# Kernel tuning notes

Measured on AMD Instinct MI355X. Metric: run time of the kernel, lower is better.

Reference implementation:

```python
import jax, jax.numpy as jnp
import numpy as np

EPS = 1e-12  # F.normalize default eps


def _l2norm(x):
    n = jnp.linalg.norm(x, axis=-1, keepdims=True)
    return x / jnp.maximum(n, EPS)


def _group_pool(x):
    # x: (b, 4, C) row-normalized features; per-group attention pooling.
    # s_i = sum_j x_i . x_j ; weights = softmax_i(s) ; pooled = sum_i w_i x_i
    s = jnp.einsum('bic,bjc->bi', x, x)          # (b, 4)
    w = jax.nn.softmax(s, axis=1)                 # (b, 4)
    return jnp.einsum('bi,bic->bc', w, x)         # (b, C)


def setup_inputs() -> dict:
    key = jax.random.key(0)
    k1, k2 = jax.random.split(key)
    N, C = 16384, 1024
    x1 = jax.random.normal(k1, (N, C), dtype=jnp.float32)
    x2 = jax.random.normal(k2, (N, C), dtype=jnp.float32)
    return {"x1": x1, "x2": x2}


def reference(x1, x2):
    b = x2.shape[0] // 4
    C = x1.shape[1]
    x1n = _l2norm(x1).reshape(b, 4, C)
    x2n = _l2norm(x2).reshape(b, 4, C)
    p1 = _l2norm(_group_pool(x1n))                # (b, C)
    p2 = _l2norm(_group_pool(x2n))                # (b, C)
    center_loss = jnp.mean(jnp.linalg.norm(p1 - p2, axis=1))
    sim = p1 @ p2.T                               # (b, b)
    diag = jnp.arange(b)
    # cross_entropy(sim, arange) and cross_entropy(sim.T, arange)
    loss_t = -jnp.mean(jax.nn.log_softmax(sim, axis=1)[diag, diag])
    loss_i = -jnp.mean(jax.nn.log_softmax(sim, axis=0)[diag, diag])
    return (loss_t + loss_i + center_loss, p1, p2)
```

## Files before the change

kernel.cpp:

```cpp
#include <hip/hip_runtime.h>
#include <hip/hip_bf16.h>

#define BGRP 4096
#define CDIM 1024

typedef __attribute__((ext_vector_type(8))) short bf16x8;
typedef __attribute__((ext_vector_type(4))) float f32x4;
typedef __attribute__((ext_vector_type(4))) unsigned short u16x4;

__device__ __forceinline__ unsigned short f2bf(float x) {
    __hip_bfloat16 h = __float2bfloat16(x);
    unsigned short u;
    __builtin_memcpy(&u, &h, 2);
    return u;
}

__device__ __forceinline__ void gload16(const void* g, void* l) {
    __builtin_amdgcn_global_load_lds(
        (const __attribute__((address_space(1))) unsigned int*)g,
        (__attribute__((address_space(3))) unsigned int*)l, 16, 0, 0);
}

__device__ __forceinline__ void group_coefs(const float* d, float* coef) {
    float D[4][4];
    int c = 0;
    #pragma unroll
    for (int i = 0; i < 4; ++i)
        #pragma unroll
        for (int j = i; j < 4; ++j) { D[i][j] = d[c]; D[j][i] = d[c]; ++c; }
    float inv[4];
    #pragma unroll
    for (int i = 0; i < 4; ++i) inv[i] = 1.0f / fmaxf(sqrtf(D[i][i]), 1e-12f);
    float s[4];
    #pragma unroll
    for (int i = 0; i < 4; ++i) {
        float si = 0.f;
        #pragma unroll
        for (int j = 0; j < 4; ++j) si += D[i][j] * inv[i] * inv[j];
        s[i] = si;
    }
    float m = fmaxf(fmaxf(s[0], s[1]), fmaxf(s[2], s[3]));
    float e[4], se = 0.f;
    #pragma unroll
    for (int i = 0; i < 4; ++i) { e[i] = expf(s[i] - m); se += e[i]; }
    float rse = 1.0f / se;
    #pragma unroll
    for (int i = 0; i < 4; ++i) coef[i] = e[i] * rse * inv[i];
}

__device__ __forceinline__ float wave_allsum(float t) {
    t += __shfl_xor(t, 1, 64);
    t += __shfl_xor(t, 2, 64);
    t += __shfl_xor(t, 4, 64);
    t += __shfl_xor(t, 8, 64);
    t += __shfl_xor(t, 16, 64);
    t += __shfl_xor(t, 32, 64);
    return t;
}

__global__ __launch_bounds__(256, 4) void pool_kernel(
    const float* __restrict__ x1, const float* __restrict__ x2,
    float* __restrict__ out,
    unsigned short* __restrict__ p1b, unsigned short* __restrict__ p2b,
    float* __restrict__ diag, float* __restrict__ centerArr)
{
    __shared__ float plds[2][CDIM];
    const int l    = threadIdx.x & 63;
    const int wv   = threadIdx.x >> 6;
    const int gi   = wv >> 1;
    const int isx2 = wv & 1;
    const int g    = blockIdx.x * 2 + gi;

    const float* __restrict__ x = isx2 ? x2 : x1;

    float4 a[4][4];
    #pragma unroll
    for (int i = 0; i < 4; ++i)
        #pragma unroll
        for (int w = 0; w < 4; ++w)
            a[i][w] = reinterpret_cast<const float4*>(x)[(size_t)(4 * g + i) * 256 + w * 64 + l];

    float dd[10];
    {
        int c = 0;
        #pragma unroll
        for (int i = 0; i < 4; ++i)
            #pragma unroll
            for (int j = i; j < 4; ++j) {
                float s0 = 0.f;
                #pragma unroll
                for (int w = 0; w < 4; ++w)
                    s0 += a[i][w].x * a[j][w].x + a[i][w].y * a[j][w].y
                        + a[i][w].z * a[j][w].z + a[i][w].w * a[j][w].w;
                dd[c++] = s0;
            }
    }
    #pragma unroll
    for (int v = 0; v < 10; ++v) dd[v] = wave_allsum(dd[v]);

    float coef[4];
    group_coefs(dd, coef);

    float D[4][4];
    {
        int c = 0;
        #pragma unroll
        for (int i = 0; i < 4; ++i)
            #pragma unroll
            for (int j = i; j < 4; ++j) { D[i][j] = dd[c]; D[j][i] = dd[c]; ++c; }
    }
    float n = 0.f;
    #pragma unroll
    for (int i = 0; i < 4; ++i) {
        float ti = 0.f;
        #pragma unroll
        for (int j = 0; j < 4; ++j) ti += D[i][j] * coef[j];
        n += coef[i] * ti;
    }
    const float inv = 1.0f / fmaxf(sqrtf(n), 1e-12f);

    float* pout = out + 1 + (size_t)(g + (isx2 ? BGRP : 0)) * CDIM;
    unsigned short* pb = isx2 ? (p2b ? p2b + (size_t)g * CDIM : nullptr)
                              : (p1b ? p1b + (size_t)g * CDIM : nullptr);

    float4 q[4];
    #pragma unroll
    for (int w = 0; w < 4; ++w) {
        float4 qq;
        qq.x = coef[0]*a[0][w].x + coef[1]*a[1][w].x + coef[2]*a[2][w].x + coef[3]*a[3][w].x;
        qq.y = coef[0]*a[0][w].y + coef[1]*a[1][w].y + coef[2]*a[2][w].y + coef[3]*a[3][w].y;
        qq.z = coef[0]*a[0][w].z + coef[1]*a[1][w].z + coef[2]*a[2][w].z + coef[3]*a[3][w].z;
        qq.w = coef[0]*a[0][w].w + coef[1]*a[1][w].w + coef[2]*a[2][w].w + coef[3]*a[3][w].w;
        qq.x *= inv; qq.y *= inv; qq.z *= inv; qq.w *= inv;
        q[w] = qq;
    }

    if (!isx2) {
        #pragma unroll
        for (int w = 0; w < 4; ++w)
            *reinterpret_cast<float4*>(&plds[gi][w * 256 + l * 4]) = q[w];
    }

    #pragma unroll
    for (int w = 0; w < 4; ++w) {
        const int e = w * 256 + l * 4;
        pout[e + 0] = q[w].x; pout[e + 1] = q[w].y;
        pout[e + 2] = q[w].z; pout[e + 3] = q[w].w;
        if (pb != nullptr) {
            u16x4 wb;
            wb[0] = f2bf(q[w].x); wb[1] = f2bf(q[w].y);
            wb[2] = f2bf(q[w].z); wb[3] = f2bf(q[w].w);
            *reinterpret_cast<u16x4*>(pb + e) = wb;
        }
    }

    __syncthreads();

    if (isx2) {
        float dp = 0.f;
        #pragma unroll
        for (int w = 0; w < 4; ++w) {
            float4 p1v = *reinterpret_cast<const float4*>(&plds[gi][w * 256 + l * 4]);
            dp += p1v.x * q[w].x + p1v.y * q[w].y + p1v.z * q[w].z + p1v.w * q[w].w;
        }
        dp = wave_allsum(dp);
        if (l == 0) {
            diag[g] = dp;
            centerArr[g] = sqrtf(fmaxf(2.0f - 2.0f * dp, 0.0f));
        }
    }
}

__global__ __launch_bounds__(256, 4) void sim_lds_kernel(
    const unsigned short* __restrict__ p1b, const unsigned short* __restrict__ p2b,
    float* __restrict__ rowsum, float* __restrict__ colsum)
{
    __shared__ __align__(16) unsigned char lds[32768];
    const int tid  = threadIdx.x;
    const int lane = tid & 63;
    const int wid  = tid >> 6;
    const int wm = wid >> 1, wn = wid & 1;
    const int row0 = blockIdx.y * 128;
    const int col0 = blockIdx.x * 128;
    const int lr  = lane & 15;
    const int lkb = lane >> 4;

    const int srow = lane >> 3;
    const int scol = ((lane & 7) ^ srow) << 4;
    const int ch0  = wid * 4;

    f32x4 acc[4][4];
    #pragma unroll
    for (int mi = 0; mi < 4; ++mi)
        #pragma unroll
        for (int ni = 0; ni < 4; ++ni) {
            acc[mi][ni][0] = 0.f; acc[mi][ni][1] = 0.f;
            acc[mi][ni][2] = 0.f; acc[mi][ni][3] = 0.f;
        }

    const char* A = (const char*)p1b;
    const char* B = (const char*)p2b;

    for (int kt = 0; kt < 16; ++kt) {
        const size_t kbyte = (size_t)kt * 128;
        #pragma unroll
        for (int c = 0; c < 4; ++c) {
            const int chunk = ch0 + c;
            const int r = chunk * 8 + srow;
            gload16(A + (size_t)(row0 + r) * 2048 + kbyte + scol, lds + chunk * 1024);
            gload16(B + (size_t)(col0 + r) * 2048 + kbyte + scol, lds + 16384 + chunk * 1024);
        }
        __syncthreads();

        #pragma unroll
        for (int ks = 0; ks < 2; ++ks) {
            bf16x8 af[4], bg[4];
            const int cbase = (ks * 64 + lkb * 16) ^ ((lr & 7) << 4);
            #pragma unroll
            for (int i = 0; i < 4; ++i) {
                const int ra = wm * 64 + i * 16 + lr;
                const int rb = wn * 64 + i * 16 + lr;
                af[i] = *reinterpret_cast<const bf16x8*>(lds + ra * 128 + cbase);
                bg[i] = *reinterpret_cast<const bf16x8*>(lds + 16384 + rb * 128 + cbase);
            }
            #pragma unroll
            for (int mi = 0; mi < 4; ++mi)
                #pragma unroll
                for (int ni = 0; ni < 4; ++ni)
                    acc[mi][ni] = __builtin_amdgcn_mfma_f32_16x16x32_bf16(
                        af[mi], bg[ni], acc[mi][ni], 0, 0, 0);
        }
        __syncthreads();
    }

    float rs[4][4];
    float cs[4] = {0.f, 0.f, 0.f, 0.f};
    #pragma unroll
    for (int mi = 0; mi < 4; ++mi)
        #pragma unroll
        for (int r = 0; r < 4; ++r) rs[mi][r] = 0.f;

    #pragma unroll
    for (int mi = 0; mi < 4; ++mi)
        #pragma unroll
        for (int ni = 0; ni < 4; ++ni)
            #pragma unroll
            for (int r = 0; r < 4; ++r) {
                float e = __expf(acc[mi][ni][r]);
                rs[mi][r] += e;
                cs[ni] += e;
            }

    const int wrow0 = row0 + wm * 64;
    const int wcol0 = col0 + wn * 64;
    #pragma unroll
    for (int mi = 0; mi < 4; ++mi)
        #pragma unroll
        for (int r = 0; r < 4; ++r) {
            float v = rs[mi][r];
            v += __shfl_xor(v, 1, 64);
            v += __shfl_xor(v, 2, 64);
            v += __shfl_xor(v, 4, 64);
            v += __shfl_xor(v, 8, 64);
            if (lr == 0) atomicAdd(&rowsum[wrow0 + mi * 16 + lkb * 4 + r], v);
        }
    #pragma unroll
    for (int ni = 0; ni < 4; ++ni) {
        float v = cs[ni];
        v += __shfl_xor(v, 16, 64);
        v += __shfl_xor(v, 32, 64);
        if (lkb == 0) atomicAdd(&colsum[wcol0 + ni * 16 + lr], v);
    }
}

__device__ __forceinline__ bf16x8 frag_from_f32(const float* p) {
    bf16x8 r;
    #pragma unroll
    for (int i = 0; i < 8; ++i) {
        unsigned int b = __float_as_uint(p[i]);
        b += 0x7fffu + ((b >> 16) & 1u);
        r[i] = (short)(b >> 16);
    }
    return r;
}

__global__ __launch_bounds__(256) void sim_fallback_kernel(
    const float* __restrict__ p1f, const float* __restrict__ p2f,
    float* __restrict__ rowsum, float* __restrict__ colsum)
{
    const int lane = threadIdx.x & 63;
    const int wid  = threadIdx.x >> 6;
    const int wm = wid >> 1, wn = wid & 1;
    const int row0 = blockIdx.y * 128 + wm * 64;
    const int col0 = blockIdx.x * 128 + wn * 64;
    const int lr  = lane & 15;
    const int lkb = lane >> 4;
    const int lk  = lkb * 8;

    f32x4 acc[4][4];
    #pragma unroll
    for (int mi = 0; mi < 4; ++mi)
        #pragma unroll
        for (int ni = 0; ni < 4; ++ni) {
            acc[mi][ni][0] = 0.f; acc[mi][ni][1] = 0.f;
            acc[mi][ni][2] = 0.f; acc[mi][ni][3] = 0.f;
        }

    const size_t abase = (size_t)(row0 + lr) * CDIM + lk;
    const size_t bbase = (size_t)(col0 + lr) * CDIM + lk;

    for (int k = 0; k < CDIM; k += 32) {
        bf16x8 af[4], bfr[4];
        #pragma unroll
        for (int i = 0; i < 4; ++i) {
            af[i]  = frag_from_f32(p1f + abase + (size_t)i * 16 * CDIM + k);
            bfr[i] = frag_from_f32(p2f + bbase + (size_t)i * 16 * CDIM + k);
        }
        #pragma unroll
        for (int mi = 0; mi < 4; ++mi)
            #pragma unroll
            for (int ni = 0; ni < 4; ++ni)
                acc[mi][ni] = __builtin_amdgcn_mfma_f32_16x16x32_bf16(
                    af[mi], bfr[ni], acc[mi][ni], 0, 0, 0);
    }

    float rs[4][4];
    float cs[4] = {0.f, 0.f, 0.f, 0.f};
    #pragma unroll
    for (int mi = 0; mi < 4; ++mi)
        #pragma unroll
        for (int r = 0; r < 4; ++r) rs[mi][r] = 0.f;

    #pragma unroll
    for (int mi = 0; mi < 4; ++mi)
        #pragma unroll
        for (int ni = 0; ni < 4; ++ni)
            #pragma unroll
            for (int r = 0; r < 4; ++r) {
                float e = __expf(acc[mi][ni][r]);
                rs[mi][r] += e;
                cs[ni] += e;
            }

    #pragma unroll
    for (int mi = 0; mi < 4; ++mi)
        #pragma unroll
        for (int r = 0; r < 4; ++r) {
            float v = rs[mi][r];
            v += __shfl_xor(v, 1, 64);
            v += __shfl_xor(v, 2, 64);
            v += __shfl_xor(v, 4, 64);
            v += __shfl_xor(v, 8, 64);
            if (lr == 0) atomicAdd(&rowsum[row0 + mi * 16 + lkb * 4 + r], v);
        }
    #pragma unroll
    for (int ni = 0; ni < 4; ++ni) {
        float v = cs[ni];
        v += __shfl_xor(v, 16, 64);
        v += __shfl_xor(v, 32, 64);
        if (lkb == 0) atomicAdd(&colsum[col0 + ni * 16 + lr], v);
    }
}

__global__ __launch_bounds__(256) void loss_kernel(
    const float* __restrict__ rowsum, const float* __restrict__ colsum,
    const float* __restrict__ diag, const float* __restrict__ centerArr,
    float* __restrict__ out)
{
    float part = 0.f;
    for (int i = threadIdx.x; i < BGRP; i += 256)
        part += logf(rowsum[i]) + logf(colsum[i]) - 2.0f * diag[i] + centerArr[i];
    #pragma unroll
    for (int off = 32; off > 0; off >>= 1) part += __shfl_down(part, off, 64);
    __shared__ float l4[4];
    if ((threadIdx.x & 63) == 0) l4[threadIdx.x >> 6] = part;
    __syncthreads();
    if (threadIdx.x == 0)
        out[0] = (l4[0] + l4[1] + l4[2] + l4[3]) * (1.0f / (float)BGRP);
}

extern "C" void kernel_launch(void* const* d_in, const int* in_sizes, int n_in,
                              void* d_out, int out_size, void* d_ws, size_t ws_size,
                              hipStream_t stream)
{
    const float* x1 = (const float*)d_in[0];
    const float* x2 = (const float*)d_in[1];
    float* out = (float*)d_out;

    float* rowsum    = (float*)d_ws;
    float* colsum    = rowsum + BGRP;
    float* diag      = colsum + BGRP;
    float* centerArr = diag + BGRP;
    const size_t head_floats = 4 * (size_t)BGRP;
    unsigned short* p1b = (unsigned short*)((char*)d_ws + head_floats * sizeof(float));
    unsigned short* p2b = p1b + (size_t)BGRP * CDIM;
    const size_t need = head_floats * sizeof(float) + (size_t)2 * BGRP * CDIM * sizeof(unsigned short);
    const bool use_ws = (ws_size >= need);

    hipMemsetAsync(d_ws, 0, 2 * (size_t)BGRP * sizeof(float), stream);

    pool_kernel<<<BGRP / 2, 256, 0, stream>>>(x1, x2, out,
                                              use_ws ? p1b : nullptr,
                                              use_ws ? p2b : nullptr,
                                              diag, centerArr);

    dim3 gridB(BGRP / 128, BGRP / 128);
    if (use_ws) {
        sim_lds_kernel<<<gridB, 256, 0, stream>>>(p1b, p2b, rowsum, colsum);
    } else {
        sim_fallback_kernel<<<gridB, 256, 0, stream>>>(out + 1, out + 1 + (size_t)BGRP * CDIM,
                                                       rowsum, colsum);
    }

    loss_kernel<<<1, 256, 0, stream>>>(rowsum, colsum, diag, centerArr, out);
}
```

Baseline: 86.23 us.

## Replace sim GEMM with 256x256 tile, 4-deep LDS ring pipelined kernel

Swaps the 128x128 single-buffered similarity GEMM for a 512-thread, 256x256-tile kernel that keeps a 4-slot LDS ring with two stages of global loads in flight, raising MFMA priority during compute. It also folds the rowsum/colsum memset into the pool kernel, makes the fp32 pooled-output stores nontemporal, and switches logf to __logf. The larger tiles reduce global reloads, and the prefetching hides load latency. The cost is much higher LDS use (128KB per block) and fewer blocks (256) for the device. The unswizzled 64-byte LDS rows may also cause bank conflicts.

```diff
diff --git a/kernel.cpp b/kernel.cpp
--- a/kernel.cpp
+++ b/kernel.cpp
@@ -62,8 +62,12 @@
     const float* __restrict__ x1, const float* __restrict__ x2,
     float* __restrict__ out,
     unsigned short* __restrict__ p1b, unsigned short* __restrict__ p2b,
-    float* __restrict__ diag, float* __restrict__ centerArr)
+    float* __restrict__ diag, float* __restrict__ centerArr,
+    float* __restrict__ zero8k)
 {
+    if (threadIdx.x < 4)
+        zero8k[blockIdx.x * 4 + threadIdx.x] = 0.f;
+
     __shared__ float plds[2][CDIM];
     const int l    = threadIdx.x & 63;
     const int wv   = threadIdx.x >> 6;
@@ -144,8 +148,10 @@
     #pragma unroll
     for (int w = 0; w < 4; ++w) {
         const int e = w * 256 + l * 4;
-        pout[e + 0] = q[w].x; pout[e + 1] = q[w].y;
-        pout[e + 2] = q[w].z; pout[e + 3] = q[w].w;
+        __builtin_nontemporal_store(q[w].x, pout + e + 0);
+        __builtin_nontemporal_store(q[w].y, pout + e + 1);
+        __builtin_nontemporal_store(q[w].z, pout + e + 2);
+        __builtin_nontemporal_store(q[w].w, pout + e + 3);
         if (pb != nullptr) {
             u16x4 wb;
             wb[0] = f2bf(q[w].x); wb[1] = f2bf(q[w].y);
@@ -171,105 +177,120 @@
     }
 }
 
-__global__ __launch_bounds__(256, 4) void sim_lds_kernel(
+__global__ __launch_bounds__(512, 2) void sim_ring_kernel(
     const unsigned short* __restrict__ p1b, const unsigned short* __restrict__ p2b,
     float* __restrict__ rowsum, float* __restrict__ colsum)
 {
-    __shared__ __align__(16) unsigned char lds[32768];
+    __shared__ __align__(16) unsigned char lds[131072];
     const int tid  = threadIdx.x;
     const int lane = tid & 63;
     const int wid  = tid >> 6;
-    const int wm = wid >> 1, wn = wid & 1;
-    const int row0 = blockIdx.y * 128;
-    const int col0 = blockIdx.x * 128;
-    const int lr  = lane & 15;
-    const int lkb = lane >> 4;
-
-    const int srow = lane >> 3;
-    const int scol = ((lane & 7) ^ srow) << 4;
-    const int ch0  = wid * 4;
-
-    f32x4 acc[4][4];
-    #pragma unroll
-    for (int mi = 0; mi < 4; ++mi)
-        #pragma unroll
-        for (int ni = 0; ni < 4; ++ni) {
-            acc[mi][ni][0] = 0.f; acc[mi][ni][1] = 0.f;
-            acc[mi][ni][2] = 0.f; acc[mi][ni][3] = 0.f;
-        }
+    const int wm   = wid >> 2;
+    const int wn   = wid & 3;
+    const int lr   = lane & 15;
+    const int lkb  = lane >> 4;
+    const int row0 = blockIdx.y * 256;
+    const int col0 = blockIdx.x * 256;
+
+    const int srow  = wid * 16 + (lane >> 2);
+    const int scolb = (lane & 3) * 16;
 
     const char* A = (const char*)p1b;
     const char* B = (const char*)p2b;
 
-    for (int kt = 0; kt < 16; ++kt) {
-        const size_t kbyte = (size_t)kt * 128;
-        #pragma unroll
-        for (int c = 0; c < 4; ++c) {
-            const int chunk = ch0 + c;
-            const int r = chunk * 8 + srow;
-            gload16(A + (size_t)(row0 + r) * 2048 + kbyte + scol, lds + chunk * 1024);
-            gload16(B + (size_t)(col0 + r) * 2048 + kbyte + scol, lds + 16384 + chunk * 1024);
-        }
-        __syncthreads();
-
-        #pragma unroll
-        for (int ks = 0; ks < 2; ++ks) {
-            bf16x8 af[4], bg[4];
-            const int cbase = (ks * 64 + lkb * 16) ^ ((lr & 7) << 4);
-            #pragma unroll
-            for (int i = 0; i < 4; ++i) {
-                const int ra = wm * 64 + i * 16 + lr;
-                const int rb = wn * 64 + i * 16 + lr;
-                af[i] = *reinterpret_cast<const bf16x8*>(lds + ra * 128 + cbase);
-                bg[i] = *reinterpret_cast<const bf16x8*>(lds + 16384 + rb * 128 + cbase);
+    f32x4 acc[8][4];
+    #pragma unroll
+    for (int m = 0; m < 8; ++m)
+        #pragma unroll
+        for (int n = 0; n < 4; ++n) {
+            acc[m][n][0] = 0.f; acc[m][n][1] = 0.f;
+            acc[m][n][2] = 0.f; acc[m][n][3] = 0.f;
+        }
+
+    #define STAGE(T, BUF) do {                                                  \
+        const size_t kb_ = (size_t)(T) * 64;                                    \
+        char* bb_ = (char*)lds + (BUF) * 32768;                                 \
+        _Pragma("unroll")                                                       \
+        for (int r_ = 0; r_ < 2; ++r_)                                          \
+            gload16(A + (size_t)(row0 + r_ * 128 + srow) * 2048 + kb_ + scolb,  \
+                    bb_ + r_ * 8192 + wid * 1024 + lane * 16);                  \
+        _Pragma("unroll")                                                       \
+        for (int r_ = 0; r_ < 2; ++r_)                                          \
+            gload16(B + (size_t)(col0 + r_ * 128 + srow) * 2048 + kb_ + scolb,  \
+                    bb_ + 16384 + r_ * 8192 + wid * 1024 + lane * 16);          \
+    } while (0)
+
+    STAGE(0, 0);
+    STAGE(1, 1);
+
+    for (int t = 0; t < 32; ++t) {
+        if (t < 31) { asm volatile("s_waitcnt vmcnt(4)" ::: "memory"); }
+        else        { asm volatile("s_waitcnt vmcnt(0)" ::: "memory"); }
+        __builtin_amdgcn_sched_barrier(0);
+        __builtin_amdgcn_s_barrier();
+
+        if (t + 2 < 32) STAGE(t + 2, (t + 2) & 3);
+
+        const char* bb = (const char*)lds + (t & 3) * 32768;
+        bf16x8 af[8], bg[4];
+        #pragma unroll
+        for (int m = 0; m < 8; ++m)
+            af[m] = *reinterpret_cast<const bf16x8*>(
+                bb + (wm * 128 + m * 16 + lr) * 64 + lkb * 16);
+        #pragma unroll
+        for (int n = 0; n < 4; ++n)
+            bg[n] = *reinterpret_cast<const bf16x8*>(
+                bb + 16384 + (wn * 64 + n * 16 + lr) * 64 + lkb * 16);
+
+        __builtin_amdgcn_s_barrier();
+        __builtin_amdgcn_s_setprio(1);
+        #pragma unroll
+        for (int m = 0; m < 8; ++m)
+            #pragma unroll
+            for (int n = 0; n < 4; ++n)
+                acc[m][n] = __builtin_amdgcn_mfma_f32_16x16x32_bf16(
+                    af[m], bg[n], acc[m][n], 0, 0, 0);
+        __builtin_amdgcn_s_setprio(0);
+    }
+    #undef STAGE
+
+    float rs[8][4];
+    float cs[4] = {0.f, 0.f, 0.f, 0.f};
+    #pragma unroll
+    for (int m = 0; m < 8; ++m)
+        #pragma unroll
+        for (int rr = 0; rr < 4; ++rr) rs[m][rr] = 0.f;
+
+    #pragma unroll
+    for (int m = 0; m < 8; ++m)
+        #pragma unroll
+        for (int n = 0; n < 4; ++n)
+            #pragma unroll
+            for (int rr = 0; rr < 4; ++rr) {
+                float e = __expf(acc[m][n][rr]);
+                rs[m][rr] += e;
+                cs[n] += e;
             }
-            #pragma unroll
-            for (int mi = 0; mi < 4; ++mi)
-                #pragma unroll
-                for (int ni = 0; ni < 4; ++ni)
-                    acc[mi][ni] = __builtin_amdgcn_mfma_f32_16x16x32_bf16(
-                        af[mi], bg[ni], acc[mi][ni], 0, 0, 0);
-        }
-        __syncthreads();
-    }
-
-    float rs[4][4];
-    float cs[4] = {0.f, 0.f, 0.f, 0.f};
-    #pragma unroll
-    for (int mi = 0; mi < 4; ++mi)
-        #pragma unroll
-        for (int r = 0; r < 4; ++r) rs[mi][r] = 0.f;
-
-    #pragma unroll
-    for (int mi = 0; mi < 4; ++mi)
-        #pragma unroll
-        for (int ni = 0; ni < 4; ++ni)
-            #pragma unroll
-            for (int r = 0; r < 4; ++r) {
-                float e = __expf(acc[mi][ni][r]);
-                rs[mi][r] += e;
-                cs[ni] += e;
-            }
-
-    const int wrow0 = row0 + wm * 64;
+
+    const int wrow0 = row0 + wm * 128;
     const int wcol0 = col0 + wn * 64;
     #pragma unroll
-    for (int mi = 0; mi < 4; ++mi)
-        #pragma unroll
-        for (int r = 0; r < 4; ++r) {
-            float v = rs[mi][r];
+    for (int m = 0; m < 8; ++m)
+        #pragma unroll
+        for (int rr = 0; rr < 4; ++rr) {
+            float v = rs[m][rr];
             v += __shfl_xor(v, 1, 64);
             v += __shfl_xor(v, 2, 64);
             v += __shfl_xor(v, 4, 64);
             v += __shfl_xor(v, 8, 64);
-            if (lr == 0) atomicAdd(&rowsum[wrow0 + mi * 16 + lkb * 4 + r], v);
-        }
-    #pragma unroll
-    for (int ni = 0; ni < 4; ++ni) {
-        float v = cs[ni];
+            if (lr == 0) atomicAdd(&rowsum[wrow0 + m * 16 + lkb * 4 + rr], v);
+        }
+    #pragma unroll
+    for (int n = 0; n < 4; ++n) {
+        float v = cs[n];
         v += __shfl_xor(v, 16, 64);
         v += __shfl_xor(v, 32, 64);
-        if (lkb == 0) atomicAdd(&colsum[wcol0 + ni * 16 + lr], v);
+        if (lkb == 0) atomicAdd(&colsum[wcol0 + n * 16 + lr], v);
     }
 }
 
@@ -369,7 +390,7 @@
 {
     float part = 0.f;
     for (int i = threadIdx.x; i < BGRP; i += 256)
-        part += logf(rowsum[i]) + logf(colsum[i]) - 2.0f * diag[i] + centerArr[i];
+        part += __logf(rowsum[i]) + __logf(colsum[i]) - 2.0f * diag[i] + centerArr[i];
     #pragma unroll
     for (int off = 32; off > 0; off >>= 1) part += __shfl_down(part, off, 64);
     __shared__ float l4[4];
@@ -397,17 +418,16 @@
     const size_t need = head_floats * sizeof(float) + (size_t)2 * BGRP * CDIM * sizeof(unsigned short);
     const bool use_ws = (ws_size >= need);
 
-    hipMemsetAsync(d_ws, 0, 2 * (size_t)BGRP * sizeof(float), stream);
-
     pool_kernel<<<BGRP / 2, 256, 0, stream>>>(x1, x2, out,
                                               use_ws ? p1b : nullptr,
                                               use_ws ? p2b : nullptr,
-                                              diag, centerArr);
-
-    dim3 gridB(BGRP / 128, BGRP / 128);
+                                              diag, centerArr, rowsum);
+
     if (use_ws) {
-        sim_lds_kernel<<<gridB, 256, 0, stream>>>(p1b, p2b, rowsum, colsum);
+        dim3 gridB(BGRP / 256, BGRP / 256);
+        sim_ring_kernel<<<gridB, 512, 0, stream>>>(p1b, p2b, rowsum, colsum);
     } else {
+        dim3 gridB(BGRP / 128, BGRP / 128);
         sim_fallback_kernel<<<gridB, 256, 0, stream>>>(out + 1, out + 1 + (size_t)BGRP * CDIM,
                                                        rowsum, colsum);
     }
```

Result: faster. 83.18 us (-3.5%).
